# Optimization experiments

Hardware: AMD Instinct MI355X
Metric: run time of the kernel (lower is better)

Reference implementation:

```python
import jax, jax.numpy as jnp
import numpy as np

N = 50000
D = 64
E = 800000
P_DROP = 0.1


def setup_inputs() -> dict:
    key = jax.random.key(0)
    k1, k2, k3, k4 = jax.random.split(key, 4)
    x = jnp.arange(N, dtype=jnp.int32)
    edge_src = jax.random.randint(k1, (E,), 0, N, dtype=jnp.int32)
    edge_dst = jax.random.randint(k2, (E,), 0, N, dtype=jnp.int32)
    # symmetric-normalization-like positive edge weights
    edge_vals = jax.random.uniform(k3, (E,), dtype=jnp.float32) / 16.0
    # xavier_uniform for Embedding(N, D)
    limit = float(np.sqrt(6.0 / (N + D)))
    embed_weight = jax.random.uniform(k4, (N, D), minval=-limit, maxval=limit, dtype=jnp.float32)
    return {"x": x, "edge_src": edge_src, "edge_dst": edge_dst,
            "edge_vals": edge_vals, "embed_weight": embed_weight}


def _spmm(edge_src, edge_dst, edge_vals, h):
    # out[i] = sum_{(j->i) in E} A[i,j] * h[j]  (gather -> scale -> scatter-add)
    msgs = edge_vals[:, None] * h[edge_src]          # [E, D]
    return jax.ops.segment_sum(msgs, edge_dst, num_segments=N)


def _dropout(key, h, p=P_DROP):
    keep = jax.random.bernoulli(key, 1.0 - p, h.shape)
    return jnp.where(keep, h / (1.0 - p), 0.0).astype(h.dtype)


def reference(x, edge_src, edge_dst, edge_vals, embed_weight):
    dk1, dk2, dk3 = jax.random.split(jax.random.key(1), 3)
    h0 = embed_weight[x]                             # [N, D] embedding lookup
    h1 = _spmm(edge_src, edge_dst, edge_vals, _dropout(dk1, h0))
    h2 = _spmm(edge_src, edge_dst, edge_vals, _dropout(dk2, h1))
    h3 = _spmm(edge_src, edge_dst, edge_vals, _dropout(dk3, h2))
    return (h0 + h1 + h2 + h3) / 4.0
```

## Files before the change

### kernel.cpp

```cpp
#include <hip/hip_runtime.h>
#include <stdint.h>

static const int kN = 50000;
static const int kD = 64;
static const int kE = 800000;
static const int kChunk = 3200;
static const int kG = kE / kChunk;
static const int kB = 196;
static const int kCapB = 6144;

#define TFR(x0, x1, r)                                    \
  {                                                       \
    x0 += x1;                                             \
    x1 = ((x1 << (r)) | (x1 >> (32 - (r))));              \
    x1 ^= x0;                                             \
  }

__host__ __device__ inline void tf2x32(uint32_t k0, uint32_t k1, uint32_t x0,
                                       uint32_t x1, uint32_t* o0, uint32_t* o1) {
  uint32_t k2 = k0 ^ k1 ^ 0x1BD11BDAu;
  x0 += k0; x1 += k1;
  TFR(x0, x1, 13) TFR(x0, x1, 15) TFR(x0, x1, 26) TFR(x0, x1, 6)
  x0 += k1; x1 += k2 + 1u;
  TFR(x0, x1, 17) TFR(x0, x1, 29) TFR(x0, x1, 16) TFR(x0, x1, 24)
  x0 += k2; x1 += k0 + 2u;
  TFR(x0, x1, 13) TFR(x0, x1, 15) TFR(x0, x1, 26) TFR(x0, x1, 6)
  x0 += k0; x1 += k1 + 3u;
  TFR(x0, x1, 17) TFR(x0, x1, 29) TFR(x0, x1, 16) TFR(x0, x1, 24)
  x0 += k1; x1 += k2 + 4u;
  TFR(x0, x1, 13) TFR(x0, x1, 15) TFR(x0, x1, 26) TFR(x0, x1, 6)
  x0 += k2; x1 += k0 + 5u;
  *o0 = x0; *o1 = x1;
}

__device__ inline float jax_dropout(float h, uint32_t k0, uint32_t k1, uint32_t idx) {
  uint32_t a, b;
  tf2x32(k0, k1, 0u, idx, &a, &b);
  uint32_t bits = a ^ b;
  float u = __uint_as_float((bits >> 9) | 0x3f800000u) - 1.0f;
  return (u < 0.9f) ? (h / 0.9f) : 0.0f;
}

__device__ inline unsigned short f2bf(float v) {
  uint32_t x = __float_as_uint(v);
  return (unsigned short)((x + 0x7fffu + ((x >> 16) & 1u)) >> 16);
}
__device__ inline float bf2f(unsigned short b) {
  return __uint_as_float(((uint32_t)b) << 16);
}

__global__ __launch_bounds__(320) void binA_k(const int* __restrict__ src,
                                              const int* __restrict__ dst,
                                              const float* __restrict__ val,
                                              int* __restrict__ locOffT,
                                              int2* __restrict__ staged) {
  __shared__ int2 buf[kChunk];
  __shared__ int hist[kB];
  __shared__ int off[kB + 1];
  __shared__ int sm[2][256];
  int c = blockIdx.x, t = threadIdx.x;
  int base = c * kChunk;
  for (int i = t; i < kB; i += 320) hist[i] = 0;
  __syncthreads();
  int2 sv[10];
  int bkt[10];
#pragma unroll
  for (int i = 0; i < 10; ++i) {
    int e = base + t + i * 320;
    int d = dst[e];
    int b = d >> 8;
    bkt[i] = b;
    sv[i] = make_int2(((d & 255) << 16) | src[e], __float_as_int(val[e]));
    atomicAdd(&hist[b], 1);
  }
  __syncthreads();
  int v = 0;
  if (t < 256) {
    v = (t < kB) ? hist[t] : 0;
    sm[0][t] = v;
  }
  __syncthreads();
  int p = 0;
  for (int o = 1; o < 256; o <<= 1) {
    if (t < 256) sm[p ^ 1][t] = sm[p][t] + ((t >= o) ? sm[p][t - o] : 0);
    __syncthreads();
    p ^= 1;
  }
  if (t < kB) off[t] = sm[p][t] - v;
  if (t == 0) off[kB] = kChunk;
  __syncthreads();
  for (int i = t; i <= kB; i += 320) locOffT[i * kG + c] = off[i];
  for (int i = t; i < kB; i += 320) hist[i] = off[i];
  __syncthreads();
#pragma unroll
  for (int i = 0; i < 10; ++i) {
    int pos = atomicAdd(&hist[bkt[i]], 1);
    buf[pos] = sv[i];
  }
  __syncthreads();
  for (int i = t; i < kChunk; i += 320) staged[base + i] = buf[i];
}

__global__ __launch_bounds__(256) void scanM_k(const int* __restrict__ locOffT,
                                               int* __restrict__ colTot) {
  __shared__ int red[256];
  int b = blockIdx.x, t = threadIdx.x;
  int v = 0;
  if (t < kG) v = locOffT[(b + 1) * kG + t] - locOffT[b * kG + t];
  red[t] = v;
  __syncthreads();
  for (int o = 128; o > 0; o >>= 1) {
    if (t < o) red[t] += red[t + o];
    __syncthreads();
  }
  if (t == 0) colTot[b] = red[0];
}

__global__ __launch_bounds__(256) void scanBB_k(const int* __restrict__ colTot,
                                                int* __restrict__ bucketBase,
                                                int* __restrict__ offsets) {
  __shared__ int sm[2][256];
  int t = threadIdx.x;
  int v = (t < kB) ? colTot[t] : 0;
  sm[0][t] = v;
  __syncthreads();
  int p = 0;
  for (int o = 1; o < 256; o <<= 1) {
    sm[p ^ 1][t] = sm[p][t] + ((t >= o) ? sm[p][t - o] : 0);
    __syncthreads();
    p ^= 1;
  }
  if (t < kB) bucketBase[t] = sm[p][t] - v;
  if (t == 0) {
    bucketBase[kB] = kE;
    offsets[kN] = kE;
  }
}

__global__ __launch_bounds__(256) void binB_k(const int2* __restrict__ staged,
                                              const int* __restrict__ locOffT,
                                              const int* __restrict__ bucketBase,
                                              int2* __restrict__ csr_sv,
                                              int* __restrict__ offsets) {
  __shared__ int2 buf[kCapB];
  __shared__ int sm[2][256];
  __shared__ int nodeA[256];
  int b = blockIdx.x, t = threadIdx.x;
  int base = bucketBase[b];
  int size = bucketBase[b + 1] - base;
  if (size > kCapB) size = kCapB;
  int myOff = 0, myCnt = 0;
  if (t < kG) {
    myOff = locOffT[b * kG + t];
    myCnt = locOffT[(b + 1) * kG + t] - myOff;
  }
  sm[0][t] = myCnt;
  __syncthreads();
  int p = 0;
  for (int o = 1; o < 256; o <<= 1) {
    sm[p ^ 1][t] = sm[p][t] + ((t >= o) ? sm[p][t - o] : 0);
    __syncthreads();
    p ^= 1;
  }
  int myPos = sm[p][t] - myCnt;
  for (int i = 0; i < myCnt; ++i) {
    int q = myPos + i;
    if (q < kCapB) buf[q] = staged[t * kChunk + myOff + i];
  }
  nodeA[t] = 0;
  __syncthreads();
  for (int i = t; i < size; i += 256) atomicAdd(&nodeA[buf[i].x >> 16], 1);
  __syncthreads();
  int nc = nodeA[t];
  sm[0][t] = nc;
  __syncthreads();
  p = 0;
  for (int o = 1; o < 256; o <<= 1) {
    sm[p ^ 1][t] = sm[p][t] + ((t >= o) ? sm[p][t - o] : 0);
    __syncthreads();
    p ^= 1;
  }
  int nOff = sm[p][t] - nc;
  int node = (b << 8) + t;
  if (node < kN) offsets[node] = base + nOff;
  nodeA[t] = nOff;
  __syncthreads();
  for (int i = t; i < size; i += 256) {
    int2 e = buf[i];
    int dl = e.x >> 16;
    int pp = atomicAdd(&nodeA[dl], 1);
    csr_sv[base + pp] = make_int2(e.x & 0xffff, e.y);
  }
}

__global__ void init_k(const int* __restrict__ x, const float* __restrict__ w,
                       float* __restrict__ acc, unsigned short* __restrict__ hB,
                       uint32_t k0, uint32_t k1) {
  int g = blockIdx.x * blockDim.x + threadIdx.x;
  if (g >= kN * kD / 4) return;
  int n = g >> 4, d4 = g & 15;
  float4 v = reinterpret_cast<const float4*>(w)[(size_t)x[n] * 16 + d4];
  reinterpret_cast<float4*>(acc)[g] = v;
  uint32_t idx = (uint32_t)g * 4u;
  ushort4 o;
  o.x = f2bf(jax_dropout(v.x, k0, k1, idx + 0));
  o.y = f2bf(jax_dropout(v.y, k0, k1, idx + 1));
  o.z = f2bf(jax_dropout(v.z, k0, k1, idx + 2));
  o.w = f2bf(jax_dropout(v.w, k0, k1, idx + 3));
  reinterpret_cast<ushort4*>(hB)[g] = o;
}

__global__ __launch_bounds__(256) void layer_k(
    const int2* __restrict__ csr_sv, const int* __restrict__ offsets,
    const unsigned short* __restrict__ hIn, float* __restrict__ acc,
    unsigned short* __restrict__ hOut, uint32_t k0, uint32_t k1, int last) {
  int gtid = blockIdx.x * blockDim.x + threadIdx.x;
  int node = gtid >> 6;
  int lane = threadIdx.x & 63;
  if (node >= kN) return;
  int beg = __builtin_amdgcn_readfirstlane(offsets[node]);
  int end = __builtin_amdgcn_readfirstlane(offsets[node + 1]);
  int deg = end - beg;
  float sum = 0.0f;
  for (int c = 0; c < deg; c += 16) {
    const int2* p = csr_sv + beg + c;
    int rem = deg - c;
    float g[16], vv[16];
#pragma unroll
    for (int j = 0; j < 16; ++j) {
      int2 sv = p[j];
      int s = (j < rem) ? sv.x : 0;
      vv[j] = (j < rem) ? __int_as_float(sv.y) : 0.0f;
      g[j] = bf2f(hIn[(s << 6) + lane]);
    }
#pragma unroll
    for (int j = 0; j < 16; ++j) sum += vv[j] * g[j];
  }
  int idx = (node << 6) + lane;
  if (last) {
    acc[idx] = (acc[idx] + sum) * 0.25f;
  } else {
    acc[idx] += sum;
    hOut[idx] = f2bf(jax_dropout(sum, k0, k1, (uint32_t)idx));
  }
}

extern "C" void kernel_launch(void* const* d_in, const int* in_sizes, int n_in,
                              void* d_out, int out_size, void* d_ws, size_t ws_size,
                              hipStream_t stream) {
  const int* x = (const int*)d_in[0];
  const int* esrc = (const int*)d_in[1];
  const int* edst = (const int*)d_in[2];
  const float* evals = (const float*)d_in[3];
  const float* w = (const float*)d_in[4];
  float* acc = (float*)d_out;

  size_t nd = (size_t)kN * kD;
  int2* staged = (int2*)d_ws;
  int2* csr_sv = staged + kE;
  unsigned short* hB0 = (unsigned short*)(csr_sv + kE + 16);
  unsigned short* hB1 = hB0 + nd;
  int* locOffT = (int*)(hB1 + nd);
  int* colTot = locOffT + (kB + 1) * kG;
  int* bucketBase = colTot + kB;
  int* offsets = bucketBase + kB + 1;

  uint32_t dk[3][2];
  for (int i = 0; i < 3; ++i) tf2x32(0u, 1u, 0u, (uint32_t)i, &dk[i][0], &dk[i][1]);

  const int T = 256;

  hipMemsetAsync(csr_sv + kE, 0, 16 * sizeof(int2), stream);
  binA_k<<<kG, 320, 0, stream>>>(esrc, edst, evals, locOffT, staged);
  scanM_k<<<kB, T, 0, stream>>>(locOffT, colTot);
  scanBB_k<<<1, T, 0, stream>>>(colTot, bucketBase, offsets);
  binB_k<<<kB, T, 0, stream>>>(staged, locOffT, bucketBase, csr_sv, offsets);

  init_k<<<(int)(nd / 4 + T - 1) / T, T, 0, stream>>>(x, w, acc, hB0, dk[0][0], dk[0][1]);

  const int gridL = (int)((nd + T - 1) / T);
  layer_k<<<gridL, T, 0, stream>>>(csr_sv, offsets, hB0, acc, hB1, dk[1][0], dk[1][1], 0);
  layer_k<<<gridL, T, 0, stream>>>(csr_sv, offsets, hB1, acc, hB0, dk[2][0], dk[2][1], 0);
  layer_k<<<gridL, T, 0, stream>>>(csr_sv, offsets, hB0, acc, hB1, 0u, 0u, 1);
}
```

Baseline: 160.5 us.

## Split SpMM by source half for L2 locality and fuse setup kernels

The CSR build now orders each node's edges by whether the source is in the lower or upper half of the node range, and records a mid offset per node. Each propagation layer then runs as two passes, one per source half. The first 512 blocks of each pass prefetch that half of the bf16 feature table so the gathers can hit in L2. The first pass stores fp32 partial sums and the second adds them and does the accumulate and dropout. Separately, the embedding init is folded into the binning kernel as extra blocks, the two scan kernels are merged into one, and the gather unroll drops from 16 to 8. The cost is twice as many layer launches, an extra partial-sum round trip through memory, and redundant prefetch reads.

```diff
diff --git a/kernel.cpp b/kernel.cpp
--- a/kernel.cpp
+++ b/kernel.cpp
@@ -8,6 +8,8 @@
 static const int kG = kE / kChunk;
 static const int kB = 196;
 static const int kCapB = 6144;
+static const int kHalf = 25000;
+static const int kInitBlocks = (kN * kD / 4 + 319) / 320;
 
 #define TFR(x0, x1, r)                                    \
   {                                                       \
@@ -49,80 +51,87 @@
   return __uint_as_float(((uint32_t)b) << 16);
 }
 
-__global__ __launch_bounds__(320) void binA_k(const int* __restrict__ src,
-                                              const int* __restrict__ dst,
-                                              const float* __restrict__ val,
-                                              int* __restrict__ locOffT,
-                                              int2* __restrict__ staged) {
-  __shared__ int2 buf[kChunk];
-  __shared__ int hist[kB];
-  __shared__ int off[kB + 1];
-  __shared__ int sm[2][256];
-  int c = blockIdx.x, t = threadIdx.x;
-  int base = c * kChunk;
-  for (int i = t; i < kB; i += 320) hist[i] = 0;
-  __syncthreads();
-  int2 sv[10];
-  int bkt[10];
+__global__ __launch_bounds__(320) void fusedA_k(
+    const int* __restrict__ esrc, const int* __restrict__ edst,
+    const float* __restrict__ evals, int* __restrict__ locOffT,
+    int2* __restrict__ staged, const int* __restrict__ x,
+    const float* __restrict__ w, float* __restrict__ acc,
+    unsigned short* __restrict__ hB, uint32_t k0, uint32_t k1) {
+  int t = threadIdx.x;
+  if (blockIdx.x < kG) {
+    __shared__ int2 buf[kChunk];
+    __shared__ int hist[kB];
+    __shared__ int off[kB + 1];
+    __shared__ int sm[2][256];
+    int c = blockIdx.x;
+    int base = c * kChunk;
+    for (int i = t; i < kB; i += 320) hist[i] = 0;
+    __syncthreads();
+    int2 sv[10];
+    int bkt[10];
 #pragma unroll
-  for (int i = 0; i < 10; ++i) {
-    int e = base + t + i * 320;
-    int d = dst[e];
-    int b = d >> 8;
-    bkt[i] = b;
-    sv[i] = make_int2(((d & 255) << 16) | src[e], __float_as_int(val[e]));
-    atomicAdd(&hist[b], 1);
-  }
-  __syncthreads();
-  int v = 0;
-  if (t < 256) {
-    v = (t < kB) ? hist[t] : 0;
-    sm[0][t] = v;
-  }
-  __syncthreads();
-  int p = 0;
-  for (int o = 1; o < 256; o <<= 1) {
-    if (t < 256) sm[p ^ 1][t] = sm[p][t] + ((t >= o) ? sm[p][t - o] : 0);
-    __syncthreads();
-    p ^= 1;
-  }
-  if (t < kB) off[t] = sm[p][t] - v;
-  if (t == 0) off[kB] = kChunk;
-  __syncthreads();
-  for (int i = t; i <= kB; i += 320) locOffT[i * kG + c] = off[i];
-  for (int i = t; i < kB; i += 320) hist[i] = off[i];
-  __syncthreads();
+    for (int i = 0; i < 10; ++i) {
+      int e = base + t + i * 320;
+      int d = edst[e];
+      int b = d >> 8;
+      bkt[i] = b;
+      sv[i] = make_int2(((d & 255) << 16) | esrc[e], __float_as_int(evals[e]));
+      atomicAdd(&hist[b], 1);
+    }
+    __syncthreads();
+    int v = 0;
+    if (t < 256) {
+      v = (t < kB) ? hist[t] : 0;
+      sm[0][t] = v;
+    }
+    __syncthreads();
+    int p = 0;
+    for (int o = 1; o < 256; o <<= 1) {
+      if (t < 256) sm[p ^ 1][t] = sm[p][t] + ((t >= o) ? sm[p][t - o] : 0);
+      __syncthreads();
+      p ^= 1;
+    }
+    if (t < kB) off[t] = sm[p][t] - v;
+    if (t == 0) off[kB] = kChunk;
+    __syncthreads();
+    for (int i = t; i <= kB; i += 320) locOffT[i * kG + c] = off[i];
+    for (int i = t; i < kB; i += 320) hist[i] = off[i];
+    __syncthreads();
 #pragma unroll
-  for (int i = 0; i < 10; ++i) {
-    int pos = atomicAdd(&hist[bkt[i]], 1);
-    buf[pos] = sv[i];
-  }
-  __syncthreads();
-  for (int i = t; i < kChunk; i += 320) staged[base + i] = buf[i];
-}
-
-__global__ __launch_bounds__(256) void scanM_k(const int* __restrict__ locOffT,
-                                               int* __restrict__ colTot) {
-  __shared__ int red[256];
-  int b = blockIdx.x, t = threadIdx.x;
-  int v = 0;
-  if (t < kG) v = locOffT[(b + 1) * kG + t] - locOffT[b * kG + t];
-  red[t] = v;
-  __syncthreads();
-  for (int o = 128; o > 0; o >>= 1) {
-    if (t < o) red[t] += red[t + o];
-    __syncthreads();
-  }
-  if (t == 0) colTot[b] = red[0];
-}
-
-__global__ __launch_bounds__(256) void scanBB_k(const int* __restrict__ colTot,
-                                                int* __restrict__ bucketBase,
-                                                int* __restrict__ offsets) {
+    for (int i = 0; i < 10; ++i) {
+      int pos = atomicAdd(&hist[bkt[i]], 1);
+      buf[pos] = sv[i];
+    }
+    __syncthreads();
+    for (int i = t; i < kChunk; i += 320) staged[base + i] = buf[i];
+  } else {
+    int gi = (blockIdx.x - kG) * 320 + t;
+    if (gi >= kN * kD / 4) return;
+    int n = gi >> 4, d4 = gi & 15;
+    float4 v = reinterpret_cast<const float4*>(w)[(size_t)x[n] * 16 + d4];
+    reinterpret_cast<float4*>(acc)[gi] = v;
+    uint32_t idx = (uint32_t)gi * 4u;
+    ushort4 o;
+    o.x = f2bf(jax_dropout(v.x, k0, k1, idx + 0));
+    o.y = f2bf(jax_dropout(v.y, k0, k1, idx + 1));
+    o.z = f2bf(jax_dropout(v.z, k0, k1, idx + 2));
+    o.w = f2bf(jax_dropout(v.w, k0, k1, idx + 3));
+    reinterpret_cast<ushort4*>(hB)[gi] = o;
+  }
+}
+
+__global__ __launch_bounds__(256) void scanAll_k(const int* __restrict__ locOffT,
+                                                 int* __restrict__ bucketBase,
+                                                 int* __restrict__ offsets) {
   __shared__ int sm[2][256];
   int t = threadIdx.x;
-  int v = (t < kB) ? colTot[t] : 0;
-  sm[0][t] = v;
+  int tot = 0;
+  if (t < kB) {
+    const int* r0 = locOffT + t * kG;
+    const int* r1 = locOffT + (t + 1) * kG;
+    for (int c = 0; c < kG; ++c) tot += r1[c] - r0[c];
+  }
+  sm[0][t] = tot;
   __syncthreads();
   int p = 0;
   for (int o = 1; o < 256; o <<= 1) {
@@ -130,7 +139,7 @@
     __syncthreads();
     p ^= 1;
   }
-  if (t < kB) bucketBase[t] = sm[p][t] - v;
+  if (t < kB) bucketBase[t] = sm[p][t] - tot;
   if (t == 0) {
     bucketBase[kB] = kE;
     offsets[kN] = kE;
@@ -141,10 +150,11 @@
                                               const int* __restrict__ locOffT,
                                               const int* __restrict__ bucketBase,
                                               int2* __restrict__ csr_sv,
-                                              int* __restrict__ offsets) {
+                                              int* __restrict__ offsets,
+                                              int* __restrict__ mid) {
   __shared__ int2 buf[kCapB];
   __shared__ int sm[2][256];
-  __shared__ int nodeA[256];
+  __shared__ int cnt[512];
   int b = blockIdx.x, t = threadIdx.x;
   int base = bucketBase[b];
   int size = bucketBase[b + 1] - base;
@@ -167,12 +177,18 @@
     int q = myPos + i;
     if (q < kCapB) buf[q] = staged[t * kChunk + myOff + i];
   }
-  nodeA[t] = 0;
-  __syncthreads();
-  for (int i = t; i < size; i += 256) atomicAdd(&nodeA[buf[i].x >> 16], 1);
-  __syncthreads();
-  int nc = nodeA[t];
-  sm[0][t] = nc;
+  cnt[t] = 0;
+  cnt[t + 256] = 0;
+  __syncthreads();
+  for (int i = t; i < size; i += 256) {
+    int2 e = buf[i];
+    int key = ((e.x >> 16) << 1) | (((e.x & 0xffff) >= kHalf) ? 1 : 0);
+    atomicAdd(&cnt[key], 1);
+  }
+  __syncthreads();
+  int a0 = cnt[2 * t], a1 = cnt[2 * t + 1];
+  int s = a0 + a1;
+  sm[0][t] = s;
   __syncthreads();
   p = 0;
   for (int o = 1; o < 256; o <<= 1) {
@@ -180,68 +196,72 @@
     __syncthreads();
     p ^= 1;
   }
-  int nOff = sm[p][t] - nc;
+  int basePair = sm[p][t] - s;
   int node = (b << 8) + t;
-  if (node < kN) offsets[node] = base + nOff;
-  nodeA[t] = nOff;
+  if (node < kN) {
+    offsets[node] = base + basePair;
+    mid[node] = base + basePair + a0;
+  }
+  cnt[2 * t] = basePair;
+  cnt[2 * t + 1] = basePair + a0;
   __syncthreads();
   for (int i = t; i < size; i += 256) {
     int2 e = buf[i];
-    int dl = e.x >> 16;
-    int pp = atomicAdd(&nodeA[dl], 1);
-    csr_sv[base + pp] = make_int2(e.x & 0xffff, e.y);
-  }
-}
-
-__global__ void init_k(const int* __restrict__ x, const float* __restrict__ w,
-                       float* __restrict__ acc, unsigned short* __restrict__ hB,
-                       uint32_t k0, uint32_t k1) {
-  int g = blockIdx.x * blockDim.x + threadIdx.x;
-  if (g >= kN * kD / 4) return;
-  int n = g >> 4, d4 = g & 15;
-  float4 v = reinterpret_cast<const float4*>(w)[(size_t)x[n] * 16 + d4];
-  reinterpret_cast<float4*>(acc)[g] = v;
-  uint32_t idx = (uint32_t)g * 4u;
-  ushort4 o;
-  o.x = f2bf(jax_dropout(v.x, k0, k1, idx + 0));
-  o.y = f2bf(jax_dropout(v.y, k0, k1, idx + 1));
-  o.z = f2bf(jax_dropout(v.z, k0, k1, idx + 2));
-  o.w = f2bf(jax_dropout(v.w, k0, k1, idx + 3));
-  reinterpret_cast<ushort4*>(hB)[g] = o;
-}
-
-__global__ __launch_bounds__(256) void layer_k(
-    const int2* __restrict__ csr_sv, const int* __restrict__ offsets,
-    const unsigned short* __restrict__ hIn, float* __restrict__ acc,
-    unsigned short* __restrict__ hOut, uint32_t k0, uint32_t k1, int last) {
+    int s16 = e.x & 0xffff;
+    int key = ((e.x >> 16) << 1) | ((s16 >= kHalf) ? 1 : 0);
+    int pp = atomicAdd(&cnt[key], 1);
+    csr_sv[base + pp] = make_int2(s16, e.y);
+  }
+}
+
+__global__ __launch_bounds__(256) void layerH_k(
+    const int2* __restrict__ csr_sv, const int* __restrict__ lo,
+    const int* __restrict__ hi, const unsigned short* __restrict__ hIn,
+    float* __restrict__ partial, float* __restrict__ acc,
+    unsigned short* __restrict__ hOut, uint32_t k0, uint32_t k1,
+    int phase, int last) {
+  if (blockIdx.x < 512) {
+    const uint4* pf = reinterpret_cast<const uint4*>(hIn + (size_t)phase * kHalf * kD);
+    int slice = blockIdx.x >> 3;
+    for (int i = threadIdx.x; i < 3125; i += 256) {
+      uint4 v = pf[slice * 3125 + i];
+      asm volatile("" ::"v"(v.x), "v"(v.y), "v"(v.z), "v"(v.w));
+    }
+  }
   int gtid = blockIdx.x * blockDim.x + threadIdx.x;
   int node = gtid >> 6;
   int lane = threadIdx.x & 63;
   if (node >= kN) return;
-  int beg = __builtin_amdgcn_readfirstlane(offsets[node]);
-  int end = __builtin_amdgcn_readfirstlane(offsets[node + 1]);
-  int deg = end - beg;
+  int beg = __builtin_amdgcn_readfirstlane(lo[node]);
+  int end = __builtin_amdgcn_readfirstlane(hi[node]);
   float sum = 0.0f;
-  for (int c = 0; c < deg; c += 16) {
-    const int2* p = csr_sv + beg + c;
-    int rem = deg - c;
-    float g[16], vv[16];
+  for (int c = beg; c < end; c += 8) {
+    const int2* p = csr_sv + c;
+    int rem = end - c;
+    float g[8], vv[8];
 #pragma unroll
-    for (int j = 0; j < 16; ++j) {
+    for (int j = 0; j < 8; ++j) {
       int2 sv = p[j];
       int s = (j < rem) ? sv.x : 0;
       vv[j] = (j < rem) ? __int_as_float(sv.y) : 0.0f;
       g[j] = bf2f(hIn[(s << 6) + lane]);
     }
 #pragma unroll
-    for (int j = 0; j < 16; ++j) sum += vv[j] * g[j];
+    for (int j = 0; j < 8; ++j) sum += vv[j] * g[j];
   }
   int idx = (node << 6) + lane;
-  if (last) {
-    acc[idx] = (acc[idx] + sum) * 0.25f;
+  if (phase == 0) {
+    __builtin_nontemporal_store(sum, &partial[idx]);
   } else {
-    acc[idx] += sum;
-    hOut[idx] = f2bf(jax_dropout(sum, k0, k1, (uint32_t)idx));
+    sum += __builtin_nontemporal_load(&partial[idx]);
+    float a = __builtin_nontemporal_load(&acc[idx]);
+    if (last) {
+      __builtin_nontemporal_store((a + sum) * 0.25f, &acc[idx]);
+    } else {
+      __builtin_nontemporal_store(a + sum, &acc[idx]);
+      __builtin_nontemporal_store(f2bf(jax_dropout(sum, k0, k1, (uint32_t)idx)),
+                                  &hOut[idx]);
+    }
   }
 }
 
@@ -260,26 +280,31 @@
   int2* csr_sv = staged + kE;
   unsigned short* hB0 = (unsigned short*)(csr_sv + kE + 16);
   unsigned short* hB1 = hB0 + nd;
-  int* locOffT = (int*)(hB1 + nd);
-  int* colTot = locOffT + (kB + 1) * kG;
-  int* bucketBase = colTot + kB;
+  float* partial = (float*)(hB1 + nd);
+  int* locOffT = (int*)(partial + nd);
+  int* bucketBase = locOffT + (kB + 1) * kG;
   int* offsets = bucketBase + kB + 1;
+  int* mid = offsets + kN + 1;
 
   uint32_t dk[3][2];
   for (int i = 0; i < 3; ++i) tf2x32(0u, 1u, 0u, (uint32_t)i, &dk[i][0], &dk[i][1]);
 
-  const int T = 256;
-
-  hipMemsetAsync(csr_sv + kE, 0, 16 * sizeof(int2), stream);
-  binA_k<<<kG, 320, 0, stream>>>(esrc, edst, evals, locOffT, staged);
-  scanM_k<<<kB, T, 0, stream>>>(locOffT, colTot);
-  scanBB_k<<<1, T, 0, stream>>>(colTot, bucketBase, offsets);
-  binB_k<<<kB, T, 0, stream>>>(staged, locOffT, bucketBase, csr_sv, offsets);
-
-  init_k<<<(int)(nd / 4 + T - 1) / T, T, 0, stream>>>(x, w, acc, hB0, dk[0][0], dk[0][1]);
-
-  const int gridL = (int)((nd + T - 1) / T);
-  layer_k<<<gridL, T, 0, stream>>>(csr_sv, offsets, hB0, acc, hB1, dk[1][0], dk[1][1], 0);
-  layer_k<<<gridL, T, 0, stream>>>(csr_sv, offsets, hB1, acc, hB0, dk[2][0], dk[2][1], 0);
-  layer_k<<<gridL, T, 0, stream>>>(csr_sv, offsets, hB0, acc, hB1, 0u, 0u, 1);
-}
+  fusedA_k<<<kG + kInitBlocks, 320, 0, stream>>>(esrc, edst, evals, locOffT, staged,
+                                                 x, w, acc, hB0, dk[0][0], dk[0][1]);
+  scanAll_k<<<1, 256, 0, stream>>>(locOffT, bucketBase, offsets);
+  binB_k<<<kB, 256, 0, stream>>>(staged, locOffT, bucketBase, csr_sv, offsets, mid);
+
+  const int gridL = (kN * kD) / 256;
+  layerH_k<<<gridL, 256, 0, stream>>>(csr_sv, offsets, mid, hB0, partial, acc, hB1,
+                                      dk[1][0], dk[1][1], 0, 0);
+  layerH_k<<<gridL, 256, 0, stream>>>(csr_sv, mid, offsets + 1, hB0, partial, acc, hB1,
+                                      dk[1][0], dk[1][1], 1, 0);
+  layerH_k<<<gridL, 256, 0, stream>>>(csr_sv, offsets, mid, hB1, partial, acc, hB0,
+                                      dk[2][0], dk[2][1], 0, 0);
+  layerH_k<<<gridL, 256, 0, stream>>>(csr_sv, mid, offsets + 1, hB1, partial, acc, hB0,
+                                      dk[2][0], dk[2][1], 1, 0);
+  layerH_k<<<gridL, 256, 0, stream>>>(csr_sv, offsets, mid, hB0, partial, acc, hB1,
+                                      0u, 0u, 0, 1);
+  layerH_k<<<gridL, 256, 0, stream>>>(csr_sv, mid, offsets + 1, hB0, partial, acc, hB1,
+                                      0u, 0u, 1, 1);
+}
```

Result: slower. 207.9 us (+29.5%).

## Fuse edge binning with embedding init and merge bucket scans into one kernel

Applied to the files above, without the earlier changes.

The first binning pass and the embedding/dropout init kernel now run in one launch: the first kG blocks do binning and the remaining blocks do init. The two-step bucket total and scan kernels are replaced by a single-block kernel where each thread serially sums its bucket row before a block scan. The memset of the CSR padding is dropped, and the layer kernels use nontemporal loads and stores for the accumulator and output. The aim is to remove launch overhead and small serialized kernels. The cost is a longer serial loop in one block, and layer loads past the last edge now read uninitialized padding, which is masked.

```diff
diff --git a/kernel.cpp b/kernel.cpp
--- a/kernel.cpp
+++ b/kernel.cpp
@@ -8,6 +8,7 @@
 static const int kG = kE / kChunk;
 static const int kB = 196;
 static const int kCapB = 6144;
+static const int kInitBlocks = (kN * kD / 4 + 319) / 320;
 
 #define TFR(x0, x1, r)                                    \
   {                                                       \
@@ -49,80 +50,87 @@
   return __uint_as_float(((uint32_t)b) << 16);
 }
 
-__global__ __launch_bounds__(320) void binA_k(const int* __restrict__ src,
-                                              const int* __restrict__ dst,
-                                              const float* __restrict__ val,
-                                              int* __restrict__ locOffT,
-                                              int2* __restrict__ staged) {
-  __shared__ int2 buf[kChunk];
-  __shared__ int hist[kB];
-  __shared__ int off[kB + 1];
-  __shared__ int sm[2][256];
-  int c = blockIdx.x, t = threadIdx.x;
-  int base = c * kChunk;
-  for (int i = t; i < kB; i += 320) hist[i] = 0;
-  __syncthreads();
-  int2 sv[10];
-  int bkt[10];
-#pragma unroll
-  for (int i = 0; i < 10; ++i) {
-    int e = base + t + i * 320;
-    int d = dst[e];
-    int b = d >> 8;
-    bkt[i] = b;
-    sv[i] = make_int2(((d & 255) << 16) | src[e], __float_as_int(val[e]));
-    atomicAdd(&hist[b], 1);
-  }
-  __syncthreads();
-  int v = 0;
-  if (t < 256) {
-    v = (t < kB) ? hist[t] : 0;
-    sm[0][t] = v;
-  }
-  __syncthreads();
-  int p = 0;
-  for (int o = 1; o < 256; o <<= 1) {
-    if (t < 256) sm[p ^ 1][t] = sm[p][t] + ((t >= o) ? sm[p][t - o] : 0);
-    __syncthreads();
-    p ^= 1;
-  }
-  if (t < kB) off[t] = sm[p][t] - v;
-  if (t == 0) off[kB] = kChunk;
-  __syncthreads();
-  for (int i = t; i <= kB; i += 320) locOffT[i * kG + c] = off[i];
-  for (int i = t; i < kB; i += 320) hist[i] = off[i];
-  __syncthreads();
-#pragma unroll
-  for (int i = 0; i < 10; ++i) {
-    int pos = atomicAdd(&hist[bkt[i]], 1);
-    buf[pos] = sv[i];
-  }
-  __syncthreads();
-  for (int i = t; i < kChunk; i += 320) staged[base + i] = buf[i];
-}
-
-__global__ __launch_bounds__(256) void scanM_k(const int* __restrict__ locOffT,
-                                               int* __restrict__ colTot) {
-  __shared__ int red[256];
-  int b = blockIdx.x, t = threadIdx.x;
-  int v = 0;
-  if (t < kG) v = locOffT[(b + 1) * kG + t] - locOffT[b * kG + t];
-  red[t] = v;
-  __syncthreads();
-  for (int o = 128; o > 0; o >>= 1) {
-    if (t < o) red[t] += red[t + o];
-    __syncthreads();
-  }
-  if (t == 0) colTot[b] = red[0];
-}
-
-__global__ __launch_bounds__(256) void scanBB_k(const int* __restrict__ colTot,
-                                                int* __restrict__ bucketBase,
-                                                int* __restrict__ offsets) {
+__global__ __launch_bounds__(320) void fusedA_k(
+    const int* __restrict__ esrc, const int* __restrict__ edst,
+    const float* __restrict__ evals, int* __restrict__ locOffT,
+    int2* __restrict__ staged, const int* __restrict__ x,
+    const float* __restrict__ w, float* __restrict__ acc,
+    unsigned short* __restrict__ hB, uint32_t k0, uint32_t k1) {
+  int t = threadIdx.x;
+  if (blockIdx.x < kG) {
+    __shared__ int2 buf[kChunk];
+    __shared__ int hist[kB];
+    __shared__ int off[kB + 1];
+    __shared__ int sm[2][256];
+    int c = blockIdx.x;
+    int base = c * kChunk;
+    for (int i = t; i < kB; i += 320) hist[i] = 0;
+    __syncthreads();
+    int2 sv[10];
+    int bkt[10];
+#pragma unroll
+    for (int i = 0; i < 10; ++i) {
+      int e = base + t + i * 320;
+      int d = edst[e];
+      int b = d >> 8;
+      bkt[i] = b;
+      sv[i] = make_int2(((d & 255) << 16) | esrc[e], __float_as_int(evals[e]));
+      atomicAdd(&hist[b], 1);
+    }
+    __syncthreads();
+    int v = 0;
+    if (t < 256) {
+      v = (t < kB) ? hist[t] : 0;
+      sm[0][t] = v;
+    }
+    __syncthreads();
+    int p = 0;
+    for (int o = 1; o < 256; o <<= 1) {
+      if (t < 256) sm[p ^ 1][t] = sm[p][t] + ((t >= o) ? sm[p][t - o] : 0);
+      __syncthreads();
+      p ^= 1;
+    }
+    if (t < kB) off[t] = sm[p][t] - v;
+    if (t == 0) off[kB] = kChunk;
+    __syncthreads();
+    for (int i = t; i <= kB; i += 320) locOffT[i * kG + c] = off[i];
+    for (int i = t; i < kB; i += 320) hist[i] = off[i];
+    __syncthreads();
+#pragma unroll
+    for (int i = 0; i < 10; ++i) {
+      int pos = atomicAdd(&hist[bkt[i]], 1);
+      buf[pos] = sv[i];
+    }
+    __syncthreads();
+    for (int i = t; i < kChunk; i += 320) staged[base + i] = buf[i];
+  } else {
+    int gi = (blockIdx.x - kG) * 320 + t;
+    if (gi >= kN * kD / 4) return;
+    int n = gi >> 4, d4 = gi & 15;
+    float4 v = reinterpret_cast<const float4*>(w)[(size_t)x[n] * 16 + d4];
+    reinterpret_cast<float4*>(acc)[gi] = v;
+    uint32_t idx = (uint32_t)gi * 4u;
+    ushort4 o;
+    o.x = f2bf(jax_dropout(v.x, k0, k1, idx + 0));
+    o.y = f2bf(jax_dropout(v.y, k0, k1, idx + 1));
+    o.z = f2bf(jax_dropout(v.z, k0, k1, idx + 2));
+    o.w = f2bf(jax_dropout(v.w, k0, k1, idx + 3));
+    reinterpret_cast<ushort4*>(hB)[gi] = o;
+  }
+}
+
+__global__ __launch_bounds__(256) void scanAll_k(const int* __restrict__ locOffT,
+                                                 int* __restrict__ bucketBase,
+                                                 int* __restrict__ offsets) {
   __shared__ int sm[2][256];
   int t = threadIdx.x;
-  int v = (t < kB) ? colTot[t] : 0;
-  sm[0][t] = v;
+  int tot = 0;
+  if (t < kB) {
+    const int* r0 = locOffT + t * kG;
+    const int* r1 = locOffT + (t + 1) * kG;
+    for (int c = 0; c < kG; ++c) tot += r1[c] - r0[c];
+  }
+  sm[0][t] = tot;
   __syncthreads();
   int p = 0;
   for (int o = 1; o < 256; o <<= 1) {
@@ -130,7 +138,7 @@
     __syncthreads();
     p ^= 1;
   }
-  if (t < kB) bucketBase[t] = sm[p][t] - v;
+  if (t < kB) bucketBase[t] = sm[p][t] - tot;
   if (t == 0) {
     bucketBase[kB] = kE;
     offsets[kN] = kE;
@@ -193,23 +201,6 @@
   }
 }
 
-__global__ void init_k(const int* __restrict__ x, const float* __restrict__ w,
-                       float* __restrict__ acc, unsigned short* __restrict__ hB,
-                       uint32_t k0, uint32_t k1) {
-  int g = blockIdx.x * blockDim.x + threadIdx.x;
-  if (g >= kN * kD / 4) return;
-  int n = g >> 4, d4 = g & 15;
-  float4 v = reinterpret_cast<const float4*>(w)[(size_t)x[n] * 16 + d4];
-  reinterpret_cast<float4*>(acc)[g] = v;
-  uint32_t idx = (uint32_t)g * 4u;
-  ushort4 o;
-  o.x = f2bf(jax_dropout(v.x, k0, k1, idx + 0));
-  o.y = f2bf(jax_dropout(v.y, k0, k1, idx + 1));
-  o.z = f2bf(jax_dropout(v.z, k0, k1, idx + 2));
-  o.w = f2bf(jax_dropout(v.w, k0, k1, idx + 3));
-  reinterpret_cast<ushort4*>(hB)[g] = o;
-}
-
 __global__ __launch_bounds__(256) void layer_k(
     const int2* __restrict__ csr_sv, const int* __restrict__ offsets,
     const unsigned short* __restrict__ hIn, float* __restrict__ acc,
@@ -237,11 +228,13 @@
     for (int j = 0; j < 16; ++j) sum += vv[j] * g[j];
   }
   int idx = (node << 6) + lane;
+  float a = __builtin_nontemporal_load(&acc[idx]);
   if (last) {
-    acc[idx] = (acc[idx] + sum) * 0.25f;
+    __builtin_nontemporal_store((a + sum) * 0.25f, &acc[idx]);
   } else {
-    acc[idx] += sum;
-    hOut[idx] = f2bf(jax_dropout(sum, k0, k1, (uint32_t)idx));
+    __builtin_nontemporal_store(a + sum, &acc[idx]);
+    __builtin_nontemporal_store(f2bf(jax_dropout(sum, k0, k1, (uint32_t)idx)),
+                                &hOut[idx]);
   }
 }
 
@@ -261,25 +254,22 @@
   unsigned short* hB0 = (unsigned short*)(csr_sv + kE + 16);
   unsigned short* hB1 = hB0 + nd;
   int* locOffT = (int*)(hB1 + nd);
-  int* colTot = locOffT + (kB + 1) * kG;
-  int* bucketBase = colTot + kB;
+  int* bucketBase = locOffT + (kB + 1) * kG;
   int* offsets = bucketBase + kB + 1;
 
   uint32_t dk[3][2];
   for (int i = 0; i < 3; ++i) tf2x32(0u, 1u, 0u, (uint32_t)i, &dk[i][0], &dk[i][1]);
 
-  const int T = 256;
-
-  hipMemsetAsync(csr_sv + kE, 0, 16 * sizeof(int2), stream);
-  binA_k<<<kG, 320, 0, stream>>>(esrc, edst, evals, locOffT, staged);
-  scanM_k<<<kB, T, 0, stream>>>(locOffT, colTot);
-  scanBB_k<<<1, T, 0, stream>>>(colTot, bucketBase, offsets);
-  binB_k<<<kB, T, 0, stream>>>(staged, locOffT, bucketBase, csr_sv, offsets);
-
-  init_k<<<(int)(nd / 4 + T - 1) / T, T, 0, stream>>>(x, w, acc, hB0, dk[0][0], dk[0][1]);
-
-  const int gridL = (int)((nd + T - 1) / T);
-  layer_k<<<gridL, T, 0, stream>>>(csr_sv, offsets, hB0, acc, hB1, dk[1][0], dk[1][1], 0);
-  layer_k<<<gridL, T, 0, stream>>>(csr_sv, offsets, hB1, acc, hB0, dk[2][0], dk[2][1], 0);
-  layer_k<<<gridL, T, 0, stream>>>(csr_sv, offsets, hB0, acc, hB1, 0u, 0u, 1);
-}
+  fusedA_k<<<kG + kInitBlocks, 320, 0, stream>>>(esrc, edst, evals, locOffT, staged,
+                                                 x, w, acc, hB0, dk[0][0], dk[0][1]);
+  scanAll_k<<<1, 256, 0, stream>>>(locOffT, bucketBase, offsets);
+  binB_k<<<kB, 256, 0, stream>>>(staged, locOffT, bucketBase, csr_sv, offsets);
+
+  const int gridL = (kN * kD) / 256;
+  layer_k<<<gridL, 256, 0, stream>>>(csr_sv, offsets, hB0, acc, hB1,
+                                     dk[1][0], dk[1][1], 0);
+  layer_k<<<gridL, 256, 0, stream>>>(csr_sv, offsets, hB1, acc, hB0,
+                                     dk[2][0], dk[2][1], 0);
+  layer_k<<<gridL, 256, 0, stream>>>(csr_sv, offsets, hB0, acc, hB1,
+                                     0u, 0u, 1);
+}
```

Result: no change. 160.6 us (+0.1%).
